# Optimization experiments

Measured on AMD Instinct MI355X. Metric: run time of the kernel, lower is better.

## Reference

```python
import jax, jax.numpy as jnp
import numpy as np
import math

D_MODEL = 2048
NUM_HEADS = 16
D_HEAD = D_MODEL // NUM_HEADS
ROPE_BASE = 10000.0

def _rope(t, pos):
    # t: [b, h, T, d_head]; standard rotate-half RoPE with base 10000.
    T, d = t.shape[-2], t.shape[-1]
    start = max(pos, 0)  # pos < 0 means training / position 0
    inv_freq = 1.0 / (ROPE_BASE ** (jnp.arange(0, d, 2, dtype=jnp.float32) / d))  # [d/2]
    positions = jnp.arange(start, start + T, dtype=jnp.float32)                   # [T]
    ang = positions[:, None] * inv_freq[None, :]                                  # [T, d/2]
    cos, sin = jnp.cos(ang), jnp.sin(ang)
    x1, x2 = t[..., : d // 2], t[..., d // 2 :]
    return jnp.concatenate([x1 * cos - x2 * sin, x1 * sin + x2 * cos], axis=-1)

def setup_inputs() -> dict:
    key = jax.random.key(0)
    kx, kq, kk, kv, kw = jax.random.split(key, 5)
    s = 1.0 / math.sqrt(D_MODEL)
    return {
        "x": jax.random.normal(kx, (2, 2048, D_MODEL), dtype=jnp.float32),
        "q_out": jax.random.normal(kq, (D_MODEL, D_MODEL), dtype=jnp.float32) * s,
        "k_out": jax.random.normal(kk, (D_MODEL, D_MODEL), dtype=jnp.float32) * s,
        "v_out": jax.random.normal(kv, (D_MODEL, D_MODEL), dtype=jnp.float32) * s,
        "w_out": jax.random.normal(kw, (D_MODEL, D_MODEL), dtype=jnp.float32) * s,
        "pos": 0,
    }

def reference(x, q_out, k_out, v_out, w_out, pos):
    b, t, d = x.shape
    h, dh = NUM_HEADS, D_HEAD

    def heads(y):  # [b, t, d] -> [b, h, t, dh]
        return y.reshape(b, t, h, dh).transpose(0, 2, 1, 3)

    q = _rope(heads(jnp.einsum('btd,de->bte', x, q_out)), pos)
    k = _rope(heads(jnp.einsum('btd,de->bte', x, k_out)), pos)
    v = heads(jnp.einsum('btd,de->bte', x, v_out))

    score = jnp.einsum('bhqd,bhkd->bhqk', q, k) / math.sqrt(dh)
    causal = jnp.triu(jnp.ones((t, t), dtype=bool), k=1)  # True above diagonal -> masked
    score = jnp.where(causal, -jnp.inf, score)
    weights = jax.nn.softmax(score, axis=-1)
    ctx = jnp.einsum('bhqk,bhkd->bhqd', weights, v)        # [b, h, t, dh]
    ctx = ctx.transpose(0, 2, 1, 3).reshape(b, t, d)
    return jnp.einsum('btd,de->bte', ctx, w_out)
```

## Files before the change

### kernel.cpp

```cpp
#include <hip/hip_runtime.h>
#include <hip/hip_bf16.h>
#include <math.h>

#define NH 16
#define DH 128
#define DM 2048
#define BB 2
#define TT 2048

typedef unsigned short u16;
typedef __attribute__((ext_vector_type(8))) __bf16 bf16x8;
typedef __attribute__((ext_vector_type(8))) u16 u16x8;
typedef __attribute__((ext_vector_type(4))) u16 u16x4;
typedef __attribute__((ext_vector_type(4))) float f32x4;

__device__ __forceinline__ float bf2f(u16 a){
  union { unsigned u; float f; } v; v.u = ((unsigned)a) << 16; return v.f;
}
__device__ __forceinline__ u16 f2bf(float f){
  union { float f; unsigned u; } v; v.f = f;
  unsigned r = v.u + 0x7fffu + ((v.u >> 16) & 1u);
  return (u16)(r >> 16);
}

typedef const __attribute__((address_space(1))) unsigned int* gas_p;
typedef __attribute__((address_space(3))) unsigned int* las_p;
__device__ __forceinline__ void gl_lds16(const u16* g, u16* lds_uniform_base){
  __builtin_amdgcn_global_load_lds((gas_p)(const void*)g,
                                   (las_p)(void*)lds_uniform_base, 16, 0, 0);
}

#define SB() do{ asm volatile("" ::: "memory"); \
                 __builtin_amdgcn_s_barrier();  \
                 asm volatile("" ::: "memory"); }while(0)
#define WAITV8 asm volatile("s_waitcnt vmcnt(8)" ::: "memory")
#define WAITV0 asm volatile("s_waitcnt vmcnt(0)" ::: "memory")

__global__ __launch_bounds__(256)
void cvt_f32_bf16(const float* __restrict__ src, u16* __restrict__ dst, int n4){
  const int i = blockIdx.x * 256 + threadIdx.x;
  if (i >= n4) return;
  const f32x4 v = *(const f32x4*)(src + (size_t)i * 4);
  u16x4 o;
  #pragma unroll
  for (int j = 0; j < 4; j++) o[j] = f2bf(v[j]);
  *(u16x4*)(dst + (size_t)i * 4) = o;
}

__global__ __launch_bounds__(256)
void transpose2048(const float* __restrict__ W, u16* __restrict__ Wt){
  __shared__ u16 tile[32][33];
  const int tx = threadIdx.x, ty = threadIdx.y;
  const int bx = blockIdx.x * 32, by = blockIdx.y * 32;
  #pragma unroll
  for (int i = 0; i < 32; i += 8)
    tile[ty + i][tx] = f2bf(W[(size_t)(by + ty + i) * DM + bx + tx]);
  __syncthreads();
  #pragma unroll
  for (int i = 0; i < 32; i += 8)
    Wt[(size_t)(bx + ty + i) * DM + by + tx] = tile[tx][ty + i];
}

__global__ __launch_bounds__(256)
void transpose3(const float* __restrict__ w0, const float* __restrict__ w1,
                const float* __restrict__ w2, u16* __restrict__ dst){
  __shared__ u16 tile[32][33];
  const int z = blockIdx.z;
  const float* W = (z == 0) ? w0 : (z == 1) ? w1 : w2;
  u16* Wt = dst + (size_t)z * DM * DM;
  const int tx = threadIdx.x, ty = threadIdx.y;
  const int bx = blockIdx.x * 32, by = blockIdx.y * 32;
  #pragma unroll
  for (int i = 0; i < 32; i += 8)
    tile[ty + i][tx] = f2bf(W[(size_t)(by + ty + i) * DM + bx + tx]);
  __syncthreads();
  #pragma unroll
  for (int i = 0; i < 32; i += 8)
    Wt[(size_t)(bx + ty + i) * DM + by + tx] = tile[tx][ty + i];
}

__global__ __launch_bounds__(256)
void gemm_bt(const u16* __restrict__ A, const u16* __restrict__ Bt_base,
             void* __restrict__ C0, u16* __restrict__ Ck, u16* __restrict__ Cv,
             int mode0){
  __shared__ u16 As[2][128][32];
  __shared__ u16 Bs[2][128][32];
  const int z = blockIdx.z;
  const u16* Bt = Bt_base + (size_t)z * DM * DM;
  void* C = (z == 0) ? C0 : (z == 1) ? (void*)Ck : (void*)Cv;
  const int mode = (z == 0) ? mode0 : (z == 1) ? 3 : 2;

  const int tid = threadIdx.x;
  const int wave = tid >> 6, lane = tid & 63;
  const int wm = wave & 1, wn = wave >> 1;
  const int row16 = lane & 15, quad = lane >> 4;
  const int m0 = blockIdx.x * 128, n0 = blockIdx.y * 128;

  const f32x4 zero = {0.f, 0.f, 0.f, 0.f};
  f32x4 acc[4][4];
  #pragma unroll
  for (int i = 0; i < 4; i++)
    #pragma unroll
    for (int j = 0; j < 4; j++) acc[i][j] = zero;

  const int srow = lane >> 2;
  const int scol = (lane & 3) * 8;

  for (int k0 = 0; k0 < DM; k0 += 64){
    #pragma unroll
    for (int c = 0; c < 2; c++){
      const int rbase = wave * 32 + c * 16;
      const u16* pa = A  + (size_t)(m0 + rbase + srow) * DM + k0 + scol;
      const u16* pb = Bt + (size_t)(n0 + rbase + srow) * DM + k0 + scol;
      gl_lds16(pa,      &As[0][rbase][0]);
      gl_lds16(pa + 32, &As[1][rbase][0]);
      gl_lds16(pb,      &Bs[0][rbase][0]);
      gl_lds16(pb + 32, &Bs[1][rbase][0]);
    }
    __syncthreads();
    #pragma unroll
    for (int buf = 0; buf < 2; buf++){
      bf16x8 af[4], bfr[4];
      #pragma unroll
      for (int mt = 0; mt < 4; mt++)
        af[mt] = *(const bf16x8*)&As[buf][wm * 64 + mt * 16 + row16][quad * 8];
      #pragma unroll
      for (int nt = 0; nt < 4; nt++)
        bfr[nt] = *(const bf16x8*)&Bs[buf][wn * 64 + nt * 16 + row16][quad * 8];
      #pragma unroll
      for (int mt = 0; mt < 4; mt++)
        #pragma unroll
        for (int nt = 0; nt < 4; nt++)
          acc[mt][nt] = __builtin_amdgcn_mfma_f32_16x16x32_bf16(af[mt], bfr[nt], acc[mt][nt], 0, 0, 0);
    }
    __syncthreads();
  }

  #pragma unroll
  for (int mt = 0; mt < 4; mt++){
    #pragma unroll
    for (int nt = 0; nt < 4; nt++){
      #pragma unroll
      for (int r = 0; r < 4; r++){
        const int m = m0 + wm * 64 + mt * 16 + quad * 4 + r;
        const int n = n0 + wn * 64 + nt * 16 + row16;
        const int b = m >> 11, t = m & (TT - 1);
        const int hh = n >> 7, dh = n & (DH - 1);
        if (mode == 1){
          ((u16*)C)[(((size_t)(b * NH + hh) * TT + t) * DH) + dh] = f2bf(acc[mt][nt][r]);
        } else if (mode == 3){
          const int dhs = dh ^ ((t & 7) << 3);
          ((u16*)C)[(((size_t)(b * NH + hh) * TT + t) * DH) + dhs] = f2bf(acc[mt][nt][r]);
        } else if (mode == 2){
          const int ts = (t & 63) ^ ((dh & 7) << 3);
          ((u16*)C)[(((size_t)(b * NH + hh) * 32 + (t >> 6)) * 8192) + dh * 64 + ts] = f2bf(acc[mt][nt][r]);
        } else {
          ((float*)C)[(size_t)m * DM + n] = acc[mt][nt][r];
        }
      }
    }
  }
}

__global__ __launch_bounds__(256)
void rope2(u16* __restrict__ qb, u16* __restrict__ kb, const int* __restrict__ posp){
  const int idx = blockIdx.x * 256 + threadIdx.x;
  const int pair = idx & 63;
  const int row = idx >> 6;
  const int t = row & (TT - 1);
  int p0 = *posp; if (p0 < 0) p0 = 0;
  const float tf = (float)(p0 + t);
  const size_t base = (size_t)row * DH;
  {
    const float inv = __expf(-(float)pair * (9.2103403719761836f / 64.f));
    const float a = tf * inv;
    const float sn = __sinf(a), cs = __cosf(a);
    const float q1 = bf2f(qb[base + pair]);
    const float q2 = bf2f(qb[base + 64 + pair]);
    qb[base + pair]      = f2bf(q1 * cs - q2 * sn);
    qb[base + 64 + pair] = f2bf(q1 * sn + q2 * cs);
  }
  {
    const int pl = pair ^ ((t & 7) << 3);
    const float inv = __expf(-(float)pl * (9.2103403719761836f / 64.f));
    const float a = tf * inv;
    const float sn = __sinf(a), cs = __cosf(a);
    const float k1 = bf2f(kb[base + pair]);
    const float k2 = bf2f(kb[base + 64 + pair]);
    kb[base + pair]      = f2bf(k1 * cs - k2 * sn);
    kb[base + 64 + pair] = f2bf(k1 * sn + k2 * cs);
  }
}

template<bool MASK>
__device__ __forceinline__ void attn_tile(
    int kt0, int qbase, int wave, int row16, int quad,
    const bf16x8 (&qf)[4],
    u16 (&k_s)[64][128], u16 (&vt_s)[128][64], u16 (&p_s)[4][16][72],
    f32x4 (&o_acc)[8], float (&l_acc)[4])
{
  const float scale = 0.08838834764831845f;
  const f32x4 zero = {0.f, 0.f, 0.f, 0.f};
  const int fx = (row16 & 7) << 3;
  f32x4 s_acc[4];
  #pragma unroll
  for (int nt = 0; nt < 4; nt++) s_acc[nt] = zero;
  __builtin_amdgcn_s_setprio(1);
  #pragma unroll
  for (int st = 0; st < 4; st++)
    #pragma unroll
    for (int nt = 0; nt < 4; nt++){
      const bf16x8 kf = *(const bf16x8*)&k_s[nt * 16 + row16][(st * 32 + quad * 8) ^ fx];
      s_acc[nt] = __builtin_amdgcn_mfma_f32_16x16x32_bf16(qf[st], kf, s_acc[nt], 0, 0, 0);
    }
  __builtin_amdgcn_s_setprio(0);
  #pragma unroll
  for (int r = 0; r < 4; r++){
    float ps = 0.f;
    #pragma unroll
    for (int nt = 0; nt < 4; nt++){
      float p = __expf(s_acc[nt][r] * scale);
      if (MASK){
        const int qr = qbase + quad * 4 + r;
        if (kt0 + nt * 16 + row16 > qr) p = 0.f;
      }
      ps += p;
      p_s[wave][quad * 4 + r][nt * 16 + row16] = f2bf(p);
    }
    l_acc[r] += ps;
  }
  asm volatile("" ::: "memory");

  __builtin_amdgcn_s_setprio(1);
  #pragma unroll
  for (int kk = 0; kk < 2; kk++){
    const bf16x8 pf = *(const bf16x8*)&p_s[wave][row16][kk * 32 + quad * 8];
    #pragma unroll
    for (int nd = 0; nd < 8; nd++){
      const bf16x8 vb = *(const bf16x8*)&vt_s[nd * 16 + row16][(kk * 32 + quad * 8) ^ fx];
      o_acc[nd] = __builtin_amdgcn_mfma_f32_16x16x32_bf16(pf, vb, o_acc[nd], 0, 0, 0);
    }
  }
  __builtin_amdgcn_s_setprio(0);
}

__device__ __forceinline__ void attn_pass(
    const u16* __restrict__ q, const u16* __restrict__ k,
    const u16* __restrict__ vtg, u16* __restrict__ ctx,
    int q0, int bh, int wave, int lane, int row16, int quad,
    u16 (&k_s)[2][64][128], u16 (&vt_s)[2][128][64], u16 (&p_s)[4][16][72])
{
  const size_t bho = (size_t)bh * TT * DH;
  const int qbase = q0 + wave * 16;
  const int nt = (q0 >> 6) + 1;

  bf16x8 qf[4];
  {
    const u16* qp = q + bho + (size_t)(qbase + row16) * DH + quad * 8;
    #pragma unroll
    for (int st = 0; st < 4; st++) qf[st] = *(const bf16x8*)(qp + st * 32);
  }

  float l_acc[4] = {0.f, 0.f, 0.f, 0.f};
  const f32x4 zero = {0.f, 0.f, 0.f, 0.f};
  f32x4 o_acc[8];
  #pragma unroll
  for (int i = 0; i < 8; i++) o_acc[i] = zero;

  const int kl_r = lane >> 4, kl_c = (lane & 15) * 8;
  const int vl_r = lane >> 3, vl_c = (lane & 7) * 8;

  #define ASTAGE(t, db) do{ \
    const int kt = (t) * 64; \
    _Pragma("unroll") \
    for (int i = 0; i < 4; i++){ \
      const int rb = wave * 16 + i * 4; \
      gl_lds16(k + bho + (size_t)(kt + rb + kl_r) * DH + kl_c, &k_s[db][rb][0]); \
    } \
    const u16* vpan = vtg + ((size_t)bh * 32 + (t)) * 8192; \
    _Pragma("unroll") \
    for (int i = 0; i < 4; i++){ \
      const int rb = wave * 32 + i * 8; \
      gl_lds16(vpan + (size_t)(rb + vl_r) * 64 + vl_c, &vt_s[db][rb][0]); \
    } \
  }while(0)

  ASTAGE(0, 0);
  for (int t = 0; t < nt; ++t){
    const int db = t & 1;
    if (t + 1 < nt){
      ASTAGE(t + 1, db ^ 1);
      WAITV8;
    } else {
      WAITV0;
    }
    SB();
    if (t < nt - 1)
      attn_tile<false>(t * 64, qbase, wave, row16, quad, qf, k_s[db], vt_s[db], p_s, o_acc, l_acc);
    else
      attn_tile<true >(t * 64, qbase, wave, row16, quad, qf, k_s[db], vt_s[db], p_s, o_acc, l_acc);
    SB();
  }
  #undef ASTAGE

  #pragma unroll
  for (int r = 0; r < 4; r++){
    #pragma unroll
    for (int off = 1; off < 16; off <<= 1) l_acc[r] += __shfl_xor(l_acc[r], off, 64);
  }

  const int b = bh >> 4, h = bh & 15;
  #pragma unroll
  for (int nd = 0; nd < 8; nd++){
    #pragma unroll
    for (int r = 0; r < 4; r++){
      const int qr = qbase + quad * 4 + r;
      const size_t off = ((size_t)b * TT + qr) * DM + h * DH + nd * 16 + row16;
      ctx[off] = f2bf(o_acc[nd][r] / l_acc[r]);
    }
  }
}

__global__ __launch_bounds__(256)
void attn_fwd(const u16* __restrict__ q, const u16* __restrict__ k,
              const u16* __restrict__ vtg, u16* __restrict__ ctx){
  __shared__ u16 k_s[2][64][128];
  __shared__ u16 vt_s[2][128][64];
  __shared__ u16 p_s[4][16][72];
  const int tid = threadIdx.x;
  const int wave = tid >> 6, lane = tid & 63;
  const int row16 = lane & 15, quad = lane >> 4;
  const int i = blockIdx.x;
  const int bh = blockIdx.y;

  attn_pass(q, k, vtg, ctx, (31 - i) * 64, bh, wave, lane, row16, quad, k_s, vt_s, p_s);
  attn_pass(q, k, vtg, ctx, i * 64,        bh, wave, lane, row16, quad, k_s, vt_s, p_s);
}

extern "C" void kernel_launch(void* const* d_in, const int* in_sizes, int n_in,
                              void* d_out, int out_size, void* d_ws, size_t ws_size,
                              hipStream_t stream){
  const float* x  = (const float*)d_in[0];
  const float* wq = (const float*)d_in[1];
  const float* wk = (const float*)d_in[2];
  const float* wv = (const float*)d_in[3];
  const float* wo = (const float*)d_in[4];
  const int* pos  = (const int*)d_in[5];

  char* ws = (char*)d_ws;
  const dim3 tg(64, 64), tb(32, 8);

  if (ws_size >= 92274688ull){
    u16* xb  = (u16*)ws;                  u16* cb = xb;
    u16* wt3 = (u16*)(ws + 16777216);
    u16* qb  = (u16*)(ws + 41943040);
    u16* kb  = (u16*)(ws + 58720256);
    u16* vtg = (u16*)(ws + 75497472);

    cvt_f32_bf16<<<8192, 256, 0, stream>>>(x, xb, 2097152);
    transpose3<<<dim3(64, 64, 3), tb, 0, stream>>>(wq, wk, wv, wt3);
    gemm_bt<<<dim3(32, 16, 3), 256, 0, stream>>>(xb, wt3, qb, kb, vtg, 1);
    transpose2048<<<tg, tb, 0, stream>>>(wo, wt3);
    rope2<<<16384, 256, 0, stream>>>(qb, kb, pos);
    attn_fwd<<<dim3(16, 32), 256, 0, stream>>>(qb, kb, vtg, cb);
    gemm_bt<<<dim3(32, 16, 1), 256, 0, stream>>>(cb, wt3, d_out, 0, 0, 0);
  } else {
    u16* xb  = (u16*)ws;                  u16* cb = xb;
    u16* wt  = (u16*)(ws + 16777216);
    u16* qb  = (u16*)(ws + 25165824);
    u16* kb  = (u16*)(ws + 41943040);
    u16* vtg = (u16*)(ws + 58720256);

    cvt_f32_bf16<<<8192, 256, 0, stream>>>(x, xb, 2097152);
    transpose2048<<<tg, tb, 0, stream>>>(wq, wt);
    gemm_bt<<<dim3(32, 16, 1), 256, 0, stream>>>(xb, wt, qb, 0, 0, 1);
    transpose2048<<<tg, tb, 0, stream>>>(wk, wt);
    gemm_bt<<<dim3(32, 16, 1), 256, 0, stream>>>(xb, wt, kb, 0, 0, 3);
    transpose2048<<<tg, tb, 0, stream>>>(wv, wt);
    gemm_bt<<<dim3(32, 16, 1), 256, 0, stream>>>(xb, wt, vtg, 0, 0, 2);
    rope2<<<16384, 256, 0, stream>>>(qb, kb, pos);
    attn_fwd<<<dim3(16, 32), 256, 0, stream>>>(qb, kb, vtg, cb);
    transpose2048<<<tg, tb, 0, stream>>>(wo, wt);
    gemm_bt<<<dim3(32, 16, 1), 256, 0, stream>>>(cb, wt, d_out, 0, 0, 0);
  }
}
```

Baseline: 407.9 us.

## Fuse Q RoPE into attention and merge x conversion into weight transpose

Q RoPE moves into the attention kernel, applied in registers to the loaded Q fragments, so the separate RoPE kernel now only rotates K. This removes one full read-modify-write pass over Q in global memory. The x fp32-to-bf16 conversion is folded into the weight-transpose launch as an extra z slice, saving one launch. The P scratch row pitch shrinks from 72 to 68, which changes LDS bank mapping and may affect conflicts or the alignment of the 16-byte P fragment reads.

Result: no change. 407.1 us (-0.2%).

```diff
diff --git a/kernel.cpp b/kernel.cpp
--- a/kernel.cpp
+++ b/kernel.cpp
@@ -22,6 +22,12 @@
   unsigned r = v.u + 0x7fffu + ((v.u >> 16) & 1u);
   return (u16)(r >> 16);
 }
+__device__ __forceinline__ __bf16 f2bfh(float f){
+  u16 r = f2bf(f); __bf16 h; __builtin_memcpy(&h, &r, 2); return h;
+}
+__device__ __forceinline__ float bfh2f(__bf16 h){
+  u16 r; __builtin_memcpy(&r, &h, 2); return bf2f(r);
+}
 
 typedef const __attribute__((address_space(1))) unsigned int* gas_p;
 typedef __attribute__((address_space(3))) unsigned int* las_p;
@@ -37,6 +43,53 @@
 #define WAITV0 asm volatile("s_waitcnt vmcnt(0)" ::: "memory")
 
 __global__ __launch_bounds__(256)
+void prep4(const float* __restrict__ w0, const float* __restrict__ w1,
+           const float* __restrict__ w2, const float* __restrict__ x,
+           u16* __restrict__ dst, u16* __restrict__ xb){
+  __shared__ u16 tile[32][33];
+  const int z = blockIdx.z;
+  const int tx = threadIdx.x, ty = threadIdx.y;
+  if (z == 3){
+    const int bid = blockIdx.y * 64 + blockIdx.x;
+    const int tid = ty * 32 + tx;
+    #pragma unroll
+    for (int rep = 0; rep < 2; rep++){
+      const int i = bid * 512 + rep * 256 + tid;
+      const f32x4 v = *(const f32x4*)(x + (size_t)i * 4);
+      u16x4 o;
+      #pragma unroll
+      for (int j = 0; j < 4; j++) o[j] = f2bf(v[j]);
+      *(u16x4*)(xb + (size_t)i * 4) = o;
+    }
+    return;
+  }
+  const float* W = (z == 0) ? w0 : (z == 1) ? w1 : w2;
+  u16* Wt = dst + (size_t)z * DM * DM;
+  const int bx = blockIdx.x * 32, by = blockIdx.y * 32;
+  #pragma unroll
+  for (int i = 0; i < 32; i += 8)
+    tile[ty + i][tx] = f2bf(W[(size_t)(by + ty + i) * DM + bx + tx]);
+  __syncthreads();
+  #pragma unroll
+  for (int i = 0; i < 32; i += 8)
+    Wt[(size_t)(bx + ty + i) * DM + by + tx] = tile[tx][ty + i];
+}
+
+__global__ __launch_bounds__(256)
+void transpose2048(const float* __restrict__ W, u16* __restrict__ Wt){
+  __shared__ u16 tile[32][33];
+  const int tx = threadIdx.x, ty = threadIdx.y;
+  const int bx = blockIdx.x * 32, by = blockIdx.y * 32;
+  #pragma unroll
+  for (int i = 0; i < 32; i += 8)
+    tile[ty + i][tx] = f2bf(W[(size_t)(by + ty + i) * DM + bx + tx]);
+  __syncthreads();
+  #pragma unroll
+  for (int i = 0; i < 32; i += 8)
+    Wt[(size_t)(bx + ty + i) * DM + by + tx] = tile[tx][ty + i];
+}
+
+__global__ __launch_bounds__(256)
 void cvt_f32_bf16(const float* __restrict__ src, u16* __restrict__ dst, int n4){
   const int i = blockIdx.x * 256 + threadIdx.x;
   if (i >= n4) return;
@@ -45,38 +98,6 @@
   #pragma unroll
   for (int j = 0; j < 4; j++) o[j] = f2bf(v[j]);
   *(u16x4*)(dst + (size_t)i * 4) = o;
-}
-
-__global__ __launch_bounds__(256)
-void transpose2048(const float* __restrict__ W, u16* __restrict__ Wt){
-  __shared__ u16 tile[32][33];
-  const int tx = threadIdx.x, ty = threadIdx.y;
-  const int bx = blockIdx.x * 32, by = blockIdx.y * 32;
-  #pragma unroll
-  for (int i = 0; i < 32; i += 8)
-    tile[ty + i][tx] = f2bf(W[(size_t)(by + ty + i) * DM + bx + tx]);
-  __syncthreads();
-  #pragma unroll
-  for (int i = 0; i < 32; i += 8)
-    Wt[(size_t)(bx + ty + i) * DM + by + tx] = tile[tx][ty + i];
-}
-
-__global__ __launch_bounds__(256)
-void transpose3(const float* __restrict__ w0, const float* __restrict__ w1,
-                const float* __restrict__ w2, u16* __restrict__ dst){
-  __shared__ u16 tile[32][33];
-  const int z = blockIdx.z;
-  const float* W = (z == 0) ? w0 : (z == 1) ? w1 : w2;
-  u16* Wt = dst + (size_t)z * DM * DM;
-  const int tx = threadIdx.x, ty = threadIdx.y;
-  const int bx = blockIdx.x * 32, by = blockIdx.y * 32;
-  #pragma unroll
-  for (int i = 0; i < 32; i += 8)
-    tile[ty + i][tx] = f2bf(W[(size_t)(by + ty + i) * DM + bx + tx]);
-  __syncthreads();
-  #pragma unroll
-  for (int i = 0; i < 32; i += 8)
-    Wt[(size_t)(bx + ty + i) * DM + by + tx] = tile[tx][ty + i];
 }
 
 __global__ __launch_bounds__(256)
@@ -163,7 +184,7 @@
 }
 
 __global__ __launch_bounds__(256)
-void rope2(u16* __restrict__ qb, u16* __restrict__ kb, const int* __restrict__ posp){
+void ropek(u16* __restrict__ kb, const int* __restrict__ posp){
   const int idx = blockIdx.x * 256 + threadIdx.x;
   const int pair = idx & 63;
   const int row = idx >> 6;
@@ -171,32 +192,21 @@
   int p0 = *posp; if (p0 < 0) p0 = 0;
   const float tf = (float)(p0 + t);
   const size_t base = (size_t)row * DH;
-  {
-    const float inv = __expf(-(float)pair * (9.2103403719761836f / 64.f));
-    const float a = tf * inv;
-    const float sn = __sinf(a), cs = __cosf(a);
-    const float q1 = bf2f(qb[base + pair]);
-    const float q2 = bf2f(qb[base + 64 + pair]);
-    qb[base + pair]      = f2bf(q1 * cs - q2 * sn);
-    qb[base + 64 + pair] = f2bf(q1 * sn + q2 * cs);
-  }
-  {
-    const int pl = pair ^ ((t & 7) << 3);
-    const float inv = __expf(-(float)pl * (9.2103403719761836f / 64.f));
-    const float a = tf * inv;
-    const float sn = __sinf(a), cs = __cosf(a);
-    const float k1 = bf2f(kb[base + pair]);
-    const float k2 = bf2f(kb[base + 64 + pair]);
-    kb[base + pair]      = f2bf(k1 * cs - k2 * sn);
-    kb[base + 64 + pair] = f2bf(k1 * sn + k2 * cs);
-  }
+  const int pl = pair ^ ((t & 7) << 3);
+  const float inv = __expf(-(float)pl * (9.2103403719761836f / 64.f));
+  const float a = tf * inv;
+  const float sn = __sinf(a), cs = __cosf(a);
+  const float k1 = bf2f(kb[base + pair]);
+  const float k2 = bf2f(kb[base + 64 + pair]);
+  kb[base + pair]      = f2bf(k1 * cs - k2 * sn);
+  kb[base + 64 + pair] = f2bf(k1 * sn + k2 * cs);
 }
 
 template<bool MASK>
 __device__ __forceinline__ void attn_tile(
     int kt0, int qbase, int wave, int row16, int quad,
     const bf16x8 (&qf)[4],
-    u16 (&k_s)[64][128], u16 (&vt_s)[128][64], u16 (&p_s)[4][16][72],
+    u16 (&k_s)[64][128], u16 (&vt_s)[128][64], u16 (&p_s)[4][16][68],
     f32x4 (&o_acc)[8], float (&l_acc)[4])
 {
   const float scale = 0.08838834764831845f;
@@ -247,8 +257,8 @@
 __device__ __forceinline__ void attn_pass(
     const u16* __restrict__ q, const u16* __restrict__ k,
     const u16* __restrict__ vtg, u16* __restrict__ ctx,
-    int q0, int bh, int wave, int lane, int row16, int quad,
-    u16 (&k_s)[2][64][128], u16 (&vt_s)[2][128][64], u16 (&p_s)[4][16][72])
+    int q0, int bh, int p0, int wave, int lane, int row16, int quad,
+    u16 (&k_s)[2][64][128], u16 (&vt_s)[2][128][64], u16 (&p_s)[4][16][68])
 {
   const size_t bho = (size_t)bh * TT * DH;
   const int qbase = q0 + wave * 16;
@@ -259,6 +269,22 @@
     const u16* qp = q + bho + (size_t)(qbase + row16) * DH + quad * 8;
     #pragma unroll
     for (int st = 0; st < 4; st++) qf[st] = *(const bf16x8*)(qp + st * 32);
+  }
+  {
+    const float tf = (float)(p0 + qbase + row16);
+    #pragma unroll
+    for (int st = 0; st < 2; st++){
+      #pragma unroll
+      for (int j = 0; j < 8; j++){
+        const int dh = st * 32 + quad * 8 + j;
+        const float inv = __expf(-(float)dh * (9.2103403719761836f / 64.f));
+        const float a = tf * inv;
+        const float sn = __sinf(a), cs = __cosf(a);
+        const float lo = bfh2f(qf[st][j]), hi = bfh2f(qf[st + 2][j]);
+        qf[st][j]     = f2bfh(lo * cs - hi * sn);
+        qf[st + 2][j] = f2bfh(lo * sn + hi * cs);
+      }
+    }
   }
 
   float l_acc[4] = {0.f, 0.f, 0.f, 0.f};
@@ -323,18 +349,20 @@
 
 __global__ __launch_bounds__(256)
 void attn_fwd(const u16* __restrict__ q, const u16* __restrict__ k,
-              const u16* __restrict__ vtg, u16* __restrict__ ctx){
+              const u16* __restrict__ vtg, u16* __restrict__ ctx,
+              const int* __restrict__ posp){
   __shared__ u16 k_s[2][64][128];
   __shared__ u16 vt_s[2][128][64];
-  __shared__ u16 p_s[4][16][72];
+  __shared__ u16 p_s[4][16][68];
   const int tid = threadIdx.x;
   const int wave = tid >> 6, lane = tid & 63;
   const int row16 = lane & 15, quad = lane >> 4;
   const int i = blockIdx.x;
   const int bh = blockIdx.y;
-
-  attn_pass(q, k, vtg, ctx, (31 - i) * 64, bh, wave, lane, row16, quad, k_s, vt_s, p_s);
-  attn_pass(q, k, vtg, ctx, i * 64,        bh, wave, lane, row16, quad, k_s, vt_s, p_s);
+  int p0 = *posp; if (p0 < 0) p0 = 0;
+
+  attn_pass(q, k, vtg, ctx, (31 - i) * 64, bh, p0, wave, lane, row16, quad, k_s, vt_s, p_s);
+  attn_pass(q, k, vtg, ctx, i * 64,        bh, p0, wave, lane, row16, quad, k_s, vt_s, p_s);
 }
 
 extern "C" void kernel_launch(void* const* d_in, const int* in_sizes, int n_in,
@@ -357,12 +385,11 @@
     u16* kb  = (u16*)(ws + 58720256);
     u16* vtg = (u16*)(ws + 75497472);
 
-    cvt_f32_bf16<<<8192, 256, 0, stream>>>(x, xb, 2097152);
-    transpose3<<<dim3(64, 64, 3), tb, 0, stream>>>(wq, wk, wv, wt3);
+    prep4<<<dim3(64, 64, 4), tb, 0, stream>>>(wq, wk, wv, x, wt3, xb);
     gemm_bt<<<dim3(32, 16, 3), 256, 0, stream>>>(xb, wt3, qb, kb, vtg, 1);
     transpose2048<<<tg, tb, 0, stream>>>(wo, wt3);
-    rope2<<<16384, 256, 0, stream>>>(qb, kb, pos);
-    attn_fwd<<<dim3(16, 32), 256, 0, stream>>>(qb, kb, vtg, cb);
+    ropek<<<16384, 256, 0, stream>>>(kb, pos);
+    attn_fwd<<<dim3(16, 32), 256, 0, stream>>>(qb, kb, vtg, cb, pos);
     gemm_bt<<<dim3(32, 16, 1), 256, 0, stream>>>(cb, wt3, d_out, 0, 0, 0);
   } else {
     u16* xb  = (u16*)ws;                  u16* cb = xb;
@@ -378,8 +405,8 @@
     gemm_bt<<<dim3(32, 16, 1), 256, 0, stream>>>(xb, wt, kb, 0, 0, 3);
     transpose2048<<<tg, tb, 0, stream>>>(wv, wt);
     gemm_bt<<<dim3(32, 16, 1), 256, 0, stream>>>(xb, wt, vtg, 0, 0, 2);
-    rope2<<<16384, 256, 0, stream>>>(qb, kb, pos);
-    attn_fwd<<<dim3(16, 32), 256, 0, stream>>>(qb, kb, vtg, cb);
+    ropek<<<16384, 256, 0, stream>>>(kb, pos);
+    attn_fwd<<<dim3(16, 32), 256, 0, stream>>>(qb, kb, vtg, cb, pos);
     transpose2048<<<tg, tb, 0, stream>>>(wo, wt);
     gemm_bt<<<dim3(32, 16, 1), 256, 0, stream>>>(cb, wt, d_out, 0, 0, 0);
   }
```
